# Performance work log

Hardware: AMD Instinct MI355X
Metric: run time of the kernel (lower is better)

Reference implementation:

```python
import jax, jax.numpy as jnp
import numpy as np

N_NODES = 100000
N_EDGES = 1600000
DIM = 128
N_SEEDS = 15000


def _gcn_stack(edges, x, Ws):
    """Multi-layer GCN with sym-normalized edge-list aggregation, residual, ReLU.
    edges: [2, E] int; x: [N, d] float; Ws: list of [d, d] weights."""
    n = x.shape[0]
    loop = jnp.arange(n, dtype=edges.dtype)
    src = jnp.concatenate([edges[0], loop])  # add self-loops
    dst = jnp.concatenate([edges[1], loop])
    deg = jax.ops.segment_sum(jnp.ones(src.shape, x.dtype), dst, num_segments=n)
    dinv = jax.lax.rsqrt(deg)  # deg >= 1 thanks to self-loops
    norm = dinv[src] * dinv[dst]  # [E+N]
    for W in Ws:
        h = x @ W                                   # [N, d] dense transform
        msg = norm[:, None] * h[src]                # gather + scale, [E+N, d]
        agg = jax.ops.segment_sum(msg, dst, num_segments=n)  # scatter-add
        x = jax.nn.relu(agg + h)                    # residual + activation
    return x


def setup_inputs() -> dict:
    key = jax.random.key(0)
    ks = jax.random.split(key, 8)
    scale = 1.0 / np.sqrt(DIM)
    return {
        "sr_ent_seeds": jax.random.randint(ks[0], (N_SEEDS,), 0, N_NODES),
        "tg_ent_seeds": jax.random.randint(ks[1], (N_SEEDS,), 0, N_NODES),
        "edges_sr": jax.random.randint(ks[2], (2, N_EDGES), 0, N_NODES),
        "edges_tg": jax.random.randint(ks[3], (2, N_EDGES), 0, N_NODES),
        "embedding_sr": jax.random.normal(ks[4], (N_NODES, DIM), jnp.float32),
        "embedding_tg": jax.random.normal(ks[5], (N_NODES, DIM), jnp.float32),
        "W0": jax.random.normal(ks[6], (DIM, DIM), jnp.float32) * scale,
        "W1": jax.random.normal(ks[7], (DIM, DIM), jnp.float32) * scale,
    }


def reference(sr_ent_seeds, tg_ent_seeds, edges_sr, edges_tg,
              embedding_sr, embedding_tg, W0, W1):
    Ws = [W0, W1]
    sr_ent_hid = _gcn_stack(edges_sr, embedding_sr, Ws)
    tg_ent_hid = _gcn_stack(edges_tg, embedding_tg, Ws)
    sr_seed_hid = sr_ent_hid[sr_ent_seeds]
    tg_seed_hid = tg_ent_hid[tg_ent_seeds]
    return (sr_seed_hid, tg_seed_hid, sr_ent_hid, tg_ent_hid)
```

## Files before the change

kernel.cpp:

```cpp
#include <hip/hip_runtime.h>

#define NN 100000
#define NE 1600000
#define NT (2 * NN)
#define ET (2 * NE)
#define DIM 128
#define NS 15000
#define SB2 ((NT + 255) / 256)
#define PAD 136
#define NRANGE 8
#define RSZ (NT / NRANGE)
#define CH 32
#define CI4 (ET / 4 / CH)
#define NE4 (NE / 4)

typedef __attribute__((ext_vector_type(8))) short frag_ab;
typedef __attribute__((ext_vector_type(4))) float frag_cd;
typedef __attribute__((ext_vector_type(4))) int i4;

__device__ __forceinline__ unsigned short f2bf(float f) {
    unsigned int u = __float_as_uint(f);
    u += 0x7fff + ((u >> 16) & 1);
    return (unsigned short)(u >> 16);
}
__device__ __forceinline__ float bflo(unsigned int u) { return __uint_as_float(u << 16); }
__device__ __forceinline__ float bfhi(unsigned int u) { return __uint_as_float(u & 0xffff0000u); }

__global__ __launch_bounds__(1024) void hist_k(const int* __restrict__ e_sr,
                                               const int* __restrict__ e_tg,
                                               int* __restrict__ P) {
    __shared__ int lc[RSZ];
    const int r = blockIdx.x & (NRANGE - 1);
    const int c = blockIdx.x >> 3;
    const int lo = r * RSZ;
    for (int i = threadIdx.x; i < RSZ; i += 1024) lc[i] = 0;
    __syncthreads();
    const int base = c * CI4;
    for (int v = threadIdx.x; v < CI4; v += 1024) {
        i4 d4;
        if (c < 16) {
            d4 = __builtin_nontemporal_load((const i4*)e_sr + NE4 + base + v);
        } else {
            d4 = __builtin_nontemporal_load((const i4*)e_tg + base + v);
            d4 += NN;
        }
#pragma unroll
        for (int j = 0; j < 4; ++j) {
            const int t = d4[j] - lo;
            if ((unsigned)t < RSZ) atomicAdd(&lc[t], 1);
        }
    }
    __syncthreads();
    for (int i = threadIdx.x; i < RSZ; i += 1024) P[c * NT + lo + i] = lc[i];
}

__global__ __launch_bounds__(256) void reduce_k(const int* __restrict__ P,
                                                int* __restrict__ cnt,
                                                float* __restrict__ dinv) {
    const int i = blockIdx.x * 256 + threadIdx.x;
    if (i >= NT) return;
    int s = 0;
#pragma unroll
    for (int c = 0; c < CH; ++c) s += P[c * NT + i];
    cnt[i] = s;
    dinv[i] = rsqrtf((float)(s + 1));
}

__global__ __launch_bounds__(256) void scanA_k(const int* __restrict__ cnt, int* bsum) {
    __shared__ int s[256];
    const int t = threadIdx.x;
    const int i = blockIdx.x * 256 + t;
    s[t] = (i < NT) ? cnt[i] : 0;
    __syncthreads();
    for (int off = 128; off > 0; off >>= 1) {
        if (t < off) s[t] += s[t + off];
        __syncthreads();
    }
    if (t == 0) bsum[blockIdx.x] = s[0];
}

__global__ __launch_bounds__(1024) void scanB_k(int* bsum, int* row_ptr) {
    __shared__ int s[1024];
    const int t = threadIdx.x;
    const int v = (t < SB2) ? bsum[t] : 0;
    s[t] = v;
    __syncthreads();
    for (int off = 1; off < 1024; off <<= 1) {
        int add = (t >= off) ? s[t - off] : 0;
        __syncthreads();
        s[t] += add;
        __syncthreads();
    }
    if (t < SB2) bsum[t] = s[t] - v;
    if (t == SB2 - 1) row_ptr[NT] = s[t];
}

__global__ __launch_bounds__(256) void scanC_k(const int* __restrict__ cnt,
                                               const int* __restrict__ bsum,
                                               int* row_ptr) {
    __shared__ int s[256];
    const int t = threadIdx.x;
    const int i = blockIdx.x * 256 + t;
    const int v = (i < NT) ? cnt[i] : 0;
    s[t] = v;
    __syncthreads();
    for (int off = 1; off < 256; off <<= 1) {
        int add = (t >= off) ? s[t - off] : 0;
        __syncthreads();
        s[t] += add;
        __syncthreads();
    }
    if (i < NT) row_ptr[i] = bsum[blockIdx.x] + s[t] - v;
}

__global__ __launch_bounds__(256) void base_k(int* __restrict__ P,
                                              const int* __restrict__ row_ptr) {
    const int i = blockIdx.x * 256 + threadIdx.x;
    if (i >= NT) return;
    int run = row_ptr[i];
#pragma unroll
    for (int c = 0; c < CH; ++c) {
        const int v = P[c * NT + i];
        P[c * NT + i] = run;
        run += v;
    }
}

__global__ __launch_bounds__(1024) void fillp_k(const int* __restrict__ e_sr,
                                                const int* __restrict__ e_tg,
                                                const int* __restrict__ P,
                                                int* __restrict__ csr_src) {
    __shared__ int cur[RSZ];
    const int r = blockIdx.x & (NRANGE - 1);
    const int c = blockIdx.x >> 3;
    const int lo = r * RSZ;
    for (int i = threadIdx.x; i < RSZ; i += 1024) cur[i] = P[c * NT + lo + i];
    __syncthreads();
    const int base = c * CI4;
    for (int v = threadIdx.x; v < CI4; v += 1024) {
        i4 s4, d4;
        if (c < 16) {
            s4 = __builtin_nontemporal_load((const i4*)e_sr + base + v);
            d4 = __builtin_nontemporal_load((const i4*)e_sr + NE4 + base + v);
        } else {
            s4 = __builtin_nontemporal_load((const i4*)e_tg + base + v - NE4);
            d4 = __builtin_nontemporal_load((const i4*)e_tg + base + v);
            s4 += NN;
            d4 += NN;
        }
#pragma unroll
        for (int j = 0; j < 4; ++j) {
            const int t = d4[j] - lo;
            if ((unsigned)t < RSZ) {
                const int pos = atomicAdd(&cur[t], 1);
                csr_src[pos] = s4[j];
            }
        }
    }
}

__global__ __launch_bounds__(256) void convX_k(const float* __restrict__ emb_sr,
                                               const float* __restrict__ emb_tg,
                                               unsigned short* __restrict__ xb) {
    const int i = blockIdx.x * 256 + threadIdx.x;
    if (i >= NT * 32) return;
    const int node = i >> 5;
    float4 v = (node < NN) ? ((const float4*)emb_sr)[i]
                           : ((const float4*)emb_tg)[i - NN * 32];
    ushort4 o;
    o.x = f2bf(v.x); o.y = f2bf(v.y); o.z = f2bf(v.z); o.w = f2bf(v.w);
    ((ushort4*)xb)[i] = o;
}

__global__ __launch_bounds__(256) void convW_k(const float* __restrict__ W,
                                               unsigned short* __restrict__ wt) {
    int i = blockIdx.x * 256 + threadIdx.x;
    if (i >= DIM * DIM) return;
    const int n = i & 127, k = i >> 7;
    wt[n * DIM + k] = f2bf(W[k * DIM + n]);
}

__global__ __launch_bounds__(256) void gemm_mfma_k(const unsigned short* __restrict__ Xb,
                                                   const unsigned short* __restrict__ Wt,
                                                   const float* __restrict__ dinv,
                                                   unsigned short* __restrict__ Gb) {
    __shared__ unsigned short xs[64 * PAD];
    __shared__ unsigned short ws[128 * PAD];
    const int tid = threadIdx.x;
    const int row0 = blockIdx.x * 64;

    for (int i = tid; i < 128 * 16; i += 256) {
        const int r = i >> 4, o = i & 15;
        *(uint4*)&ws[r * PAD + o * 8] = *(const uint4*)&Wt[r * DIM + o * 8];
    }
    for (int i = tid; i < 64 * 16; i += 256) {
        const int r = i >> 4, o = i & 15;
        int gr = row0 + r; if (gr >= NT) gr = NT - 1;
        *(uint4*)&xs[r * PAD + o * 8] = *(const uint4*)&Xb[gr * DIM + o * 8];
    }
    __syncthreads();

    const int wave = tid >> 6;
    const int lane = tid & 63;
    const int m = lane & 15;
    const int quad = lane >> 4;
    const int rbase = wave * 16;

    frag_cd acc[8];
#pragma unroll
    for (int ct = 0; ct < 8; ct++) acc[ct] = (frag_cd){0.f, 0.f, 0.f, 0.f};

#pragma unroll
    for (int ks = 0; ks < 4; ks++) {
        const frag_ab a = *(const frag_ab*)&xs[(rbase + m) * PAD + ks * 32 + quad * 8];
#pragma unroll
        for (int ct = 0; ct < 8; ct++) {
            const frag_ab b = *(const frag_ab*)&ws[(ct * 16 + m) * PAD + ks * 32 + quad * 8];
            acc[ct] = __builtin_amdgcn_mfma_f32_16x16x32_bf16(a, b, acc[ct], 0, 0, 0);
        }
    }

#pragma unroll
    for (int r = 0; r < 4; r++) {
        const int grow = row0 + rbase + quad * 4 + r;
        if (grow < NT) {
            const float dv = dinv[grow];
#pragma unroll
            for (int ct = 0; ct < 8; ct++)
                Gb[grow * DIM + ct * 16 + m] = f2bf(dv * acc[ct][r]);
        }
    }
}

template <bool OUT_BF16>
__global__ __launch_bounds__(256) void pull_k(const int* __restrict__ row_ptr,
                                              const int* __restrict__ csr_src,
                                              const float* __restrict__ dinv,
                                              const unsigned short* __restrict__ Gb,
                                              float* __restrict__ outf,
                                              unsigned short* __restrict__ outb) {
    const int node = (blockIdx.x * 256 + threadIdx.x) >> 6;
    if (node >= NT) return;
    const int lane = threadIdx.x & 63;
    const unsigned int* __restrict__ G2 = (const unsigned int*)Gb;

    const int beg = row_ptr[node];
    const int end = row_ptr[node + 1];
    const float d = dinv[node];
    const float sq = 1.0f / d;

    const unsigned int gu = G2[node * 64 + lane];
    float sx = bflo(gu);
    float sy = bfhi(gu);
    const float hx = sx * sq;
    const float hy = sy * sq;

    for (int base = beg; base < end; base += 64) {
        int rem = end - base; if (rem > 64) rem = 64;
        const int sl = (lane < rem) ? csr_src[base + lane] : 0;
        int j = 0;
        for (; j + 4 <= rem; j += 4) {
            const int s0 = __shfl(sl, j + 0);
            const int s1 = __shfl(sl, j + 1);
            const int s2 = __shfl(sl, j + 2);
            const int s3 = __shfl(sl, j + 3);
            const unsigned int m0 = G2[s0 * 64 + lane];
            const unsigned int m1 = G2[s1 * 64 + lane];
            const unsigned int m2 = G2[s2 * 64 + lane];
            const unsigned int m3 = G2[s3 * 64 + lane];
            sx += bflo(m0) + bflo(m1) + bflo(m2) + bflo(m3);
            sy += bfhi(m0) + bfhi(m1) + bfhi(m2) + bfhi(m3);
        }
        for (; j < rem; ++j) {
            const int s = __shfl(sl, j);
            const unsigned int mu = G2[s * 64 + lane];
            sx += bflo(mu);
            sy += bfhi(mu);
        }
    }
    const float ax = fmaxf(d * sx + hx, 0.f);
    const float ay = fmaxf(d * sy + hy, 0.f);
    if (OUT_BF16) {
        ((unsigned int*)outb)[node * 64 + lane] =
            (unsigned int)f2bf(ax) | ((unsigned int)f2bf(ay) << 16);
    } else {
        float2 o; o.x = ax; o.y = ay;
        ((float2*)outf)[node * 64 + lane] = o;
    }
}

__global__ __launch_bounds__(256) void gather_k(const int* __restrict__ seeds,
                                                const float* __restrict__ ent,
                                                float* __restrict__ out, int node_off) {
    const int gid = blockIdx.x * 256 + threadIdx.x;
    const int s = gid >> 5;
    if (s >= NS) return;
    const int q = gid & 31;
    ((float4*)out)[s * 32 + q] =
        ((const float4*)ent)[(seeds[s] + node_off) * 32 + q];
}

extern "C" void kernel_launch(void* const* d_in, const int* in_sizes, int n_in,
                              void* d_out, int out_size, void* d_ws, size_t ws_size,
                              hipStream_t stream) {
    const int* sr_seeds = (const int*)d_in[0];
    const int* tg_seeds = (const int*)d_in[1];
    const int* edges_sr = (const int*)d_in[2];
    const int* edges_tg = (const int*)d_in[3];
    const float* emb_sr = (const float*)d_in[4];
    const float* emb_tg = (const float*)d_in[5];
    const float* W0 = (const float*)d_in[6];
    const float* W1 = (const float*)d_in[7];
    float* out = (float*)d_out;

    int* cnt = (int*)d_ws;
    float* dinv = (float*)(cnt + 200704);
    int* row_ptr = (int*)(dinv + 200704);
    int* bsum = row_ptr + 200704;
    int* csr_src = bsum + 1024;
    unsigned short* wt0 = (unsigned short*)(csr_src + ET);
    unsigned short* wt1 = wt0 + DIM * DIM;
    unsigned short* hb = wt1 + DIM * DIM;
    int* P = (int*)hb;

    float* sr_seed_out = out;
    float* tg_seed_out = out + (long long)NS * DIM;
    float* ent = out + (long long)2 * NS * DIM;
    unsigned short* xb = (unsigned short*)ent;

    const int gGemm = (NT + 63) / 64;
    const int gPull = NT / 4;
    const int gElem = (NT * 32 + 255) / 256;

    convW_k<<<(DIM * DIM + 255) / 256, 256, 0, stream>>>(W0, wt0);
    convW_k<<<(DIM * DIM + 255) / 256, 256, 0, stream>>>(W1, wt1);

    hist_k<<<NRANGE * CH, 1024, 0, stream>>>(edges_sr, edges_tg, P);
    reduce_k<<<SB2, 256, 0, stream>>>(P, cnt, dinv);
    scanA_k<<<SB2, 256, 0, stream>>>(cnt, bsum);
    scanB_k<<<1, 1024, 0, stream>>>(bsum, row_ptr);
    scanC_k<<<SB2, 256, 0, stream>>>(cnt, bsum, row_ptr);
    base_k<<<SB2, 256, 0, stream>>>(P, row_ptr);
    fillp_k<<<NRANGE * CH, 1024, 0, stream>>>(edges_sr, edges_tg, P, csr_src);

    convX_k<<<gElem, 256, 0, stream>>>(emb_sr, emb_tg, xb);

    gemm_mfma_k<<<gGemm, 256, 0, stream>>>(xb, wt0, dinv, hb);
    pull_k<true><<<gPull, 256, 0, stream>>>(row_ptr, csr_src, dinv, hb, nullptr, xb);
    gemm_mfma_k<<<gGemm, 256, 0, stream>>>(xb, wt1, dinv, hb);
    pull_k<false><<<gPull, 256, 0, stream>>>(row_ptr, csr_src, dinv, hb, ent, nullptr);

    const int gSeed = (NS * 32 + 255) / 256;
    gather_k<<<gSeed, 256, 0, stream>>>(sr_seeds, ent, sr_seed_out, 0);
    gather_k<<<gSeed, 256, 0, stream>>>(tg_seeds, ent, tg_seed_out, NN);
}
```

Before: 642.3 us.

## Fuse preprocessing kernels, fold bf16 conversion into first GEMM, unroll gather

Merges degree reduction with the block-sum scan, merges the scan finish with per-chunk base offsets, and merges the two weight conversions into one launch. The first GEMM now reads the fp32 embeddings and converts them to bf16 itself, which removes the separate conversion pass and its round trip through memory. The pull loop is unrolled to eight neighbour loads per step to keep more gathers in flight, and the non-temporal hints on edge loads are dropped. The GEMM bounds checks are removed, which relies on the node count being a multiple of 64.

```diff
diff --git a/kernel.cpp b/kernel.cpp
--- a/kernel.cpp
+++ b/kernel.cpp
@@ -39,9 +39,9 @@
     for (int v = threadIdx.x; v < CI4; v += 1024) {
         i4 d4;
         if (c < 16) {
-            d4 = __builtin_nontemporal_load((const i4*)e_sr + NE4 + base + v);
+            d4 = *((const i4*)e_sr + NE4 + base + v);
         } else {
-            d4 = __builtin_nontemporal_load((const i4*)e_tg + base + v);
+            d4 = *((const i4*)e_tg + base + v);
             d4 += NN;
         }
 #pragma unroll
@@ -54,29 +54,27 @@
     for (int i = threadIdx.x; i < RSZ; i += 1024) P[c * NT + lo + i] = lc[i];
 }
 
-__global__ __launch_bounds__(256) void reduce_k(const int* __restrict__ P,
-                                                int* __restrict__ cnt,
-                                                float* __restrict__ dinv) {
-    const int i = blockIdx.x * 256 + threadIdx.x;
-    if (i >= NT) return;
-    int s = 0;
-#pragma unroll
-    for (int c = 0; c < CH; ++c) s += P[c * NT + i];
-    cnt[i] = s;
-    dinv[i] = rsqrtf((float)(s + 1));
-}
-
-__global__ __launch_bounds__(256) void scanA_k(const int* __restrict__ cnt, int* bsum) {
-    __shared__ int s[256];
+__global__ __launch_bounds__(256) void reduceA_k(const int* __restrict__ P,
+                                                 int* __restrict__ cnt,
+                                                 float* __restrict__ dinv,
+                                                 int* __restrict__ bsum) {
+    __shared__ int sh[256];
     const int t = threadIdx.x;
     const int i = blockIdx.x * 256 + t;
-    s[t] = (i < NT) ? cnt[i] : 0;
+    int s = 0;
+    if (i < NT) {
+#pragma unroll
+        for (int c = 0; c < CH; ++c) s += P[c * NT + i];
+        cnt[i] = s;
+        dinv[i] = rsqrtf((float)(s + 1));
+    }
+    sh[t] = s;
     __syncthreads();
     for (int off = 128; off > 0; off >>= 1) {
-        if (t < off) s[t] += s[t + off];
+        if (t < off) sh[t] += sh[t + off];
         __syncthreads();
     }
-    if (t == 0) bsum[blockIdx.x] = s[0];
+    if (t == 0) bsum[blockIdx.x] = sh[0];
 }
 
 __global__ __launch_bounds__(1024) void scanB_k(int* bsum, int* row_ptr) {
@@ -95,9 +93,10 @@
     if (t == SB2 - 1) row_ptr[NT] = s[t];
 }
 
-__global__ __launch_bounds__(256) void scanC_k(const int* __restrict__ cnt,
-                                               const int* __restrict__ bsum,
-                                               int* row_ptr) {
+__global__ __launch_bounds__(256) void scanCbase_k(const int* __restrict__ cnt,
+                                                   const int* __restrict__ bsum,
+                                                   int* __restrict__ row_ptr,
+                                                   int* __restrict__ P) {
     __shared__ int s[256];
     const int t = threadIdx.x;
     const int i = blockIdx.x * 256 + t;
@@ -110,19 +109,16 @@
         s[t] += add;
         __syncthreads();
     }
-    if (i < NT) row_ptr[i] = bsum[blockIdx.x] + s[t] - v;
-}
-
-__global__ __launch_bounds__(256) void base_k(int* __restrict__ P,
-                                              const int* __restrict__ row_ptr) {
-    const int i = blockIdx.x * 256 + threadIdx.x;
-    if (i >= NT) return;
-    int run = row_ptr[i];
-#pragma unroll
-    for (int c = 0; c < CH; ++c) {
-        const int v = P[c * NT + i];
-        P[c * NT + i] = run;
-        run += v;
+    if (i < NT) {
+        const int rp = bsum[blockIdx.x] + s[t] - v;
+        row_ptr[i] = rp;
+        int run = rp;
+#pragma unroll
+        for (int c = 0; c < CH; ++c) {
+            const int pv = P[c * NT + i];
+            P[c * NT + i] = run;
+            run += pv;
+        }
     }
 }
 
@@ -140,11 +136,11 @@
     for (int v = threadIdx.x; v < CI4; v += 1024) {
         i4 s4, d4;
         if (c < 16) {
-            s4 = __builtin_nontemporal_load((const i4*)e_sr + base + v);
-            d4 = __builtin_nontemporal_load((const i4*)e_sr + NE4 + base + v);
+            s4 = *((const i4*)e_sr + base + v);
+            d4 = *((const i4*)e_sr + NE4 + base + v);
         } else {
-            s4 = __builtin_nontemporal_load((const i4*)e_tg + base + v - NE4);
-            d4 = __builtin_nontemporal_load((const i4*)e_tg + base + v);
+            s4 = *((const i4*)e_tg + base + v - NE4);
+            d4 = *((const i4*)e_tg + base + v);
             s4 += NN;
             d4 += NN;
         }
@@ -159,25 +155,72 @@
     }
 }
 
-__global__ __launch_bounds__(256) void convX_k(const float* __restrict__ emb_sr,
+__global__ __launch_bounds__(256) void convW2_k(const float* __restrict__ W0,
+                                                const float* __restrict__ W1,
+                                                unsigned short* __restrict__ wt0,
+                                                unsigned short* __restrict__ wt1) {
+    int i = blockIdx.x * 256 + threadIdx.x;
+    if (i >= 2 * DIM * DIM) return;
+    const float* W = (i < DIM * DIM) ? W0 : W1;
+    unsigned short* wt = (i < DIM * DIM) ? wt0 : wt1;
+    const int ii = i & (DIM * DIM - 1);
+    const int n = ii & 127, k = ii >> 7;
+    wt[n * DIM + k] = f2bf(W[k * DIM + n]);
+}
+
+__global__ __launch_bounds__(256) void gemmE_k(const float* __restrict__ emb_sr,
                                                const float* __restrict__ emb_tg,
-                                               unsigned short* __restrict__ xb) {
-    const int i = blockIdx.x * 256 + threadIdx.x;
-    if (i >= NT * 32) return;
-    const int node = i >> 5;
-    float4 v = (node < NN) ? ((const float4*)emb_sr)[i]
-                           : ((const float4*)emb_tg)[i - NN * 32];
-    ushort4 o;
-    o.x = f2bf(v.x); o.y = f2bf(v.y); o.z = f2bf(v.z); o.w = f2bf(v.w);
-    ((ushort4*)xb)[i] = o;
-}
-
-__global__ __launch_bounds__(256) void convW_k(const float* __restrict__ W,
-                                               unsigned short* __restrict__ wt) {
-    int i = blockIdx.x * 256 + threadIdx.x;
-    if (i >= DIM * DIM) return;
-    const int n = i & 127, k = i >> 7;
-    wt[n * DIM + k] = f2bf(W[k * DIM + n]);
+                                               const unsigned short* __restrict__ Wt,
+                                               const float* __restrict__ dinv,
+                                               unsigned short* __restrict__ Gb) {
+    __shared__ unsigned short xs[64 * PAD];
+    __shared__ unsigned short ws[128 * PAD];
+    const int tid = threadIdx.x;
+    const int row0 = blockIdx.x * 64;
+
+    for (int i = tid; i < 128 * 16; i += 256) {
+        const int r = i >> 4, o = i & 15;
+        *(uint4*)&ws[r * PAD + o * 8] = *(const uint4*)&Wt[r * DIM + o * 8];
+    }
+    for (int i = tid; i < 64 * 32; i += 256) {
+        const int r = i >> 5, o = i & 31;
+        const int gr = row0 + r;
+        const float4 v = (gr < NN) ? ((const float4*)emb_sr)[gr * 32 + o]
+                                   : ((const float4*)emb_tg)[(gr - NN) * 32 + o];
+        ushort4 b;
+        b.x = f2bf(v.x); b.y = f2bf(v.y); b.z = f2bf(v.z); b.w = f2bf(v.w);
+        *(ushort4*)&xs[r * PAD + o * 4] = b;
+    }
+    __syncthreads();
+
+    const int wave = tid >> 6;
+    const int lane = tid & 63;
+    const int m = lane & 15;
+    const int quad = lane >> 4;
+    const int rbase = wave * 16;
+
+    frag_cd acc[8];
+#pragma unroll
+    for (int ct = 0; ct < 8; ct++) acc[ct] = (frag_cd){0.f, 0.f, 0.f, 0.f};
+
+#pragma unroll
+    for (int ks = 0; ks < 4; ks++) {
+        const frag_ab a = *(const frag_ab*)&xs[(rbase + m) * PAD + ks * 32 + quad * 8];
+#pragma unroll
+        for (int ct = 0; ct < 8; ct++) {
+            const frag_ab b = *(const frag_ab*)&ws[(ct * 16 + m) * PAD + ks * 32 + quad * 8];
+            acc[ct] = __builtin_amdgcn_mfma_f32_16x16x32_bf16(a, b, acc[ct], 0, 0, 0);
+        }
+    }
+
+#pragma unroll
+    for (int r = 0; r < 4; r++) {
+        const int grow = row0 + rbase + quad * 4 + r;
+        const float dv = dinv[grow];
+#pragma unroll
+        for (int ct = 0; ct < 8; ct++)
+            Gb[grow * DIM + ct * 16 + m] = f2bf(dv * acc[ct][r]);
+    }
 }
 
 __global__ __launch_bounds__(256) void gemm_mfma_k(const unsigned short* __restrict__ Xb,
@@ -195,8 +238,7 @@
     }
     for (int i = tid; i < 64 * 16; i += 256) {
         const int r = i >> 4, o = i & 15;
-        int gr = row0 + r; if (gr >= NT) gr = NT - 1;
-        *(uint4*)&xs[r * PAD + o * 8] = *(const uint4*)&Xb[gr * DIM + o * 8];
+        *(uint4*)&xs[r * PAD + o * 8] = *(const uint4*)&Xb[(row0 + r) * DIM + o * 8];
     }
     __syncthreads();
 
@@ -223,12 +265,10 @@
 #pragma unroll
     for (int r = 0; r < 4; r++) {
         const int grow = row0 + rbase + quad * 4 + r;
-        if (grow < NT) {
-            const float dv = dinv[grow];
-#pragma unroll
-            for (int ct = 0; ct < 8; ct++)
-                Gb[grow * DIM + ct * 16 + m] = f2bf(dv * acc[ct][r]);
-        }
+        const float dv = dinv[grow];
+#pragma unroll
+        for (int ct = 0; ct < 8; ct++)
+            Gb[grow * DIM + ct * 16 + m] = f2bf(dv * acc[ct][r]);
     }
 }
 
@@ -259,17 +299,27 @@
         int rem = end - base; if (rem > 64) rem = 64;
         const int sl = (lane < rem) ? csr_src[base + lane] : 0;
         int j = 0;
-        for (; j + 4 <= rem; j += 4) {
+        for (; j + 8 <= rem; j += 8) {
             const int s0 = __shfl(sl, j + 0);
             const int s1 = __shfl(sl, j + 1);
             const int s2 = __shfl(sl, j + 2);
             const int s3 = __shfl(sl, j + 3);
+            const int s4 = __shfl(sl, j + 4);
+            const int s5 = __shfl(sl, j + 5);
+            const int s6 = __shfl(sl, j + 6);
+            const int s7 = __shfl(sl, j + 7);
             const unsigned int m0 = G2[s0 * 64 + lane];
             const unsigned int m1 = G2[s1 * 64 + lane];
             const unsigned int m2 = G2[s2 * 64 + lane];
             const unsigned int m3 = G2[s3 * 64 + lane];
-            sx += bflo(m0) + bflo(m1) + bflo(m2) + bflo(m3);
-            sy += bfhi(m0) + bfhi(m1) + bfhi(m2) + bfhi(m3);
+            const unsigned int m4 = G2[s4 * 64 + lane];
+            const unsigned int m5 = G2[s5 * 64 + lane];
+            const unsigned int m6 = G2[s6 * 64 + lane];
+            const unsigned int m7 = G2[s7 * 64 + lane];
+            sx += bflo(m0) + bflo(m1) + bflo(m2) + bflo(m3)
+                + bflo(m4) + bflo(m5) + bflo(m6) + bflo(m7);
+            sy += bfhi(m0) + bfhi(m1) + bfhi(m2) + bfhi(m3)
+                + bfhi(m4) + bfhi(m5) + bfhi(m6) + bfhi(m7);
         }
         for (; j < rem; ++j) {
             const int s = __shfl(sl, j);
@@ -330,22 +380,16 @@
 
     const int gGemm = (NT + 63) / 64;
     const int gPull = NT / 4;
-    const int gElem = (NT * 32 + 255) / 256;
-
-    convW_k<<<(DIM * DIM + 255) / 256, 256, 0, stream>>>(W0, wt0);
-    convW_k<<<(DIM * DIM + 255) / 256, 256, 0, stream>>>(W1, wt1);
+
+    convW2_k<<<(2 * DIM * DIM + 255) / 256, 256, 0, stream>>>(W0, W1, wt0, wt1);
 
     hist_k<<<NRANGE * CH, 1024, 0, stream>>>(edges_sr, edges_tg, P);
-    reduce_k<<<SB2, 256, 0, stream>>>(P, cnt, dinv);
-    scanA_k<<<SB2, 256, 0, stream>>>(cnt, bsum);
+    reduceA_k<<<SB2, 256, 0, stream>>>(P, cnt, dinv, bsum);
     scanB_k<<<1, 1024, 0, stream>>>(bsum, row_ptr);
-    scanC_k<<<SB2, 256, 0, stream>>>(cnt, bsum, row_ptr);
-    base_k<<<SB2, 256, 0, stream>>>(P, row_ptr);
+    scanCbase_k<<<SB2, 256, 0, stream>>>(cnt, bsum, row_ptr, P);
     fillp_k<<<NRANGE * CH, 1024, 0, stream>>>(edges_sr, edges_tg, P, csr_src);
 
-    convX_k<<<gElem, 256, 0, stream>>>(emb_sr, emb_tg, xb);
-
-    gemm_mfma_k<<<gGemm, 256, 0, stream>>>(xb, wt0, dinv, hb);
+    gemmE_k<<<gGemm, 256, 0, stream>>>(emb_sr, emb_tg, wt0, dinv, hb);
     pull_k<true><<<gPull, 256, 0, stream>>>(row_ptr, csr_src, dinv, hb, nullptr, xb);
     gemm_mfma_k<<<gGemm, 256, 0, stream>>>(xb, wt1, dinv, hb);
     pull_k<false><<<gPull, 256, 0, stream>>>(row_ptr, csr_src, dinv, hb, ent, nullptr);
```

Result: faster. 590.3 us (-8.1%).
